# Performance work log

Hardware: AMD Instinct MI355X
Metric: run time of the kernel (lower is better)

Reference implementation:

```python
import jax, jax.numpy as jnp
import numpy as np

D_MODEL = 1024
N_HEADS = 16
D_K = D_MODEL // N_HEADS
D_FF = 4096
THETA = 10000.0
B, S = 2, 2048
EPS = 1e-5


def _trunc_normal(key, shape, fan_in, fan_out):
    std = np.sqrt(2.0 / (fan_in + fan_out))
    return std * jax.random.truncated_normal(key, -3.0, 3.0, shape, dtype=jnp.float32)


def setup_inputs() -> dict:
    key = jax.random.key(0)
    ks = jax.random.split(key, 9)
    x = jax.random.normal(ks[0], (B, S, D_MODEL), dtype=jnp.float32)
    wq = _trunc_normal(ks[1], (D_MODEL, D_MODEL), D_MODEL, D_MODEL)
    wk = _trunc_normal(ks[2], (D_MODEL, D_MODEL), D_MODEL, D_MODEL)
    wv = _trunc_normal(ks[3], (D_MODEL, D_MODEL), D_MODEL, D_MODEL)
    wo = _trunc_normal(ks[4], (D_MODEL, D_MODEL), D_MODEL, D_MODEL)
    w1 = _trunc_normal(ks[5], (D_FF, D_MODEL), D_MODEL, D_FF)
    w2 = _trunc_normal(ks[6], (D_MODEL, D_FF), D_FF, D_MODEL)
    w3 = _trunc_normal(ks[7], (D_FF, D_MODEL), D_MODEL, D_FF)
    g1 = jnp.ones((D_MODEL,), dtype=jnp.float32)
    g2 = jnp.ones((D_MODEL,), dtype=jnp.float32)
    return {"x": x, "wq": wq, "wk": wk, "wv": wv, "wo": wo,
            "w1": w1, "w2": w2, "w3": w3, "g1": g1, "g2": g2}


def _rmsnorm(x, gain):
    xf = x.astype(jnp.float32)
    rms = jnp.sqrt(jnp.mean(xf * xf, axis=-1, keepdims=True) + EPS)
    return (xf / rms * gain).astype(x.dtype)


def _rope(x):
    # x: [B, H, S, D_K]; block-diag 2x2 rotations on consecutive pairs
    s, d = x.shape[-2], x.shape[-1]
    pos = jnp.arange(s, dtype=jnp.float32)  # [S]
    k = jnp.arange(d // 2, dtype=jnp.float32)
    ang = pos[:, None] / (THETA ** (2.0 * k / d))[None, :]  # [S, d/2]
    cos, sin = jnp.cos(ang), jnp.sin(ang)
    xp = x.reshape(*x.shape[:-1], d // 2, 2)
    x0, x1 = xp[..., 0], xp[..., 1]
    r0 = cos * x0 - sin * x1
    r1 = sin * x0 + cos * x1
    return jnp.stack([r0, r1], axis=-1).reshape(x.shape)


def reference(x, wq, wk, wv, wo, w1, w2, w3, g1, g2):
    # --- attention sublayer ---
    h = _rmsnorm(x, g1)
    q = h @ wq.T
    k = h @ wk.T
    v = h @ wv.T
    def split_heads(t):
        b, s, _ = t.shape
        return t.reshape(b, s, N_HEADS, D_K).transpose(0, 2, 1, 3)  # [B,H,S,Dk]
    q, k, v = split_heads(q), split_heads(k), split_heads(v)
    q, k = _rope(q), _rope(k)
    scores = jnp.einsum('bhqd,bhkd->bhqk', q, k) / jnp.sqrt(jnp.float32(D_K))
    s = x.shape[-2]
    causal = jnp.tril(jnp.ones((s, s), dtype=bool))
    scores = jnp.where(causal, scores, -jnp.inf)
    attn = jax.nn.softmax(scores, axis=-1)
    o = jnp.einsum('bhqk,bhkd->bhqd', attn, v)
    o = o.transpose(0, 2, 1, 3).reshape(x.shape[0], s, D_MODEL)
    x = x + o @ wo.T
    # --- SwiGLU FFN sublayer ---
    h2 = _rmsnorm(x, g2)
    a = h2 @ w1.T
    gate = a * jax.nn.sigmoid(a)
    ff = (gate * (h2 @ w3.T)) @ w2.T
    return x + ff
```

## Files before the change

### kernel.cpp

```cpp
#include <hip/hip_runtime.h>
#include <hip/hip_bf16.h>
#include <cstddef>
#include <cstdint>

#define D_MODEL 1024
#define N_HEADS 16
#define D_K     64
#define D_FF    4096
#define BATCH   2
#define SEQ     2048
#define TOKENS  (BATCH * SEQ)
#define EPS     1e-5f

typedef __attribute__((ext_vector_type(8))) short short8;
typedef __attribute__((ext_vector_type(4))) float f32x4;

#define MFMA_BF16 __builtin_amdgcn_mfma_f32_16x16x32_bf16

static __device__ __forceinline__ short f2bf(float f) {
    __hip_bfloat16 h = __float2bfloat16(f);
    short s;
    __builtin_memcpy(&s, &h, 2);
    return s;
}

static __device__ __forceinline__ void async_ld16(const short* g, short* l) {
    __builtin_amdgcn_global_load_lds(
        (const __attribute__((address_space(1))) void*)g,
        (__attribute__((address_space(3))) void*)l,
        16, 0, 0);
}

__global__ __launch_bounds__(256) void cvt_weights(
    const float* wq, const float* wk, const float* wv, const float* wo,
    const float* w1, const float* w3, const float* w2, short* dst)
{
    const size_t M1 = 1 << 20;
    size_t e = ((size_t)blockIdx.x * 256 + threadIdx.x) * 4;
    const float* src;
    size_t off;
    if (e < M1)            { src = wq; off = e; }
    else if (e < 2 * M1)   { src = wk; off = e - M1; }
    else if (e < 3 * M1)   { src = wv; off = e - 2 * M1; }
    else if (e < 4 * M1)   { src = wo; off = e - 3 * M1; }
    else if (e < 12 * M1) {
        size_t r = (e - 4 * M1) >> 10;
        size_t col = e & 1023;
        size_t p = r >> 5, half = (r >> 4) & 1, idx = r & 15;
        src = half ? w3 : w1;
        off = (p * 16 + idx) * 1024 + col;
    }
    else                   { src = w2; off = e - 12 * M1; }
    float4 v = *reinterpret_cast<const float4*>(src + off);
    short4 o;
    o.x = f2bf(v.x); o.y = f2bf(v.y); o.z = f2bf(v.z); o.w = f2bf(v.w);
    *reinterpret_cast<short4*>(dst + e) = o;
}

__global__ __launch_bounds__(256) void rmsnorm_kernel(
    const float* __restrict__ x, const float* __restrict__ g,
    __hip_bfloat16* __restrict__ out)
{
    int row = blockIdx.x;
    int tid = threadIdx.x;
    int lane = tid & 63, wave = tid >> 6;
    const float4* xv = reinterpret_cast<const float4*>(x + (size_t)row * D_MODEL);
    float4 v = xv[tid];
    float ss = v.x * v.x + v.y * v.y + v.z * v.z + v.w * v.w;
#pragma unroll
    for (int m = 1; m < 64; m <<= 1) ss += __shfl_xor(ss, m, 64);
    __shared__ float red[4];
    if (lane == 0) red[wave] = ss;
    __syncthreads();
    float tot = red[0] + red[1] + red[2] + red[3];
    float inv = 1.0f / sqrtf(tot * (1.0f / D_MODEL) + EPS);
    float4 gv = reinterpret_cast<const float4*>(g)[tid];
    size_t base = (size_t)row * D_MODEL + (size_t)tid * 4;
    out[base + 0] = __float2bfloat16(v.x * inv * gv.x);
    out[base + 1] = __float2bfloat16(v.y * inv * gv.y);
    out[base + 2] = __float2bfloat16(v.z * inv * gv.z);
    out[base + 3] = __float2bfloat16(v.w * inv * gv.w);
}

__global__ __launch_bounds__(256) void resid_norm_kernel(
    const float* __restrict__ x, const float* __restrict__ P,
    const float* __restrict__ g, float* __restrict__ out,
    __hip_bfloat16* __restrict__ h)
{
    int row = blockIdx.x;
    int tid = threadIdx.x;
    int lane = tid & 63, wave = tid >> 6;
    size_t base = (size_t)row * D_MODEL + (size_t)tid * 4;
    float4 v  = *reinterpret_cast<const float4*>(x + base);
    float4 p0 = *reinterpret_cast<const float4*>(P + base);
    float4 p1 = *reinterpret_cast<const float4*>(P + (size_t)TOKENS * D_MODEL + base);
    v.x += p0.x + p1.x; v.y += p0.y + p1.y;
    v.z += p0.z + p1.z; v.w += p0.w + p1.w;
    *reinterpret_cast<float4*>(out + base) = v;
    float ss = v.x * v.x + v.y * v.y + v.z * v.z + v.w * v.w;
#pragma unroll
    for (int m = 1; m < 64; m <<= 1) ss += __shfl_xor(ss, m, 64);
    __shared__ float red[4];
    if (lane == 0) red[wave] = ss;
    __syncthreads();
    float tot = red[0] + red[1] + red[2] + red[3];
    float inv = 1.0f / sqrtf(tot * (1.0f / D_MODEL) + EPS);
    float4 gv = reinterpret_cast<const float4*>(g)[tid];
    h[base + 0] = __float2bfloat16(v.x * inv * gv.x);
    h[base + 1] = __float2bfloat16(v.y * inv * gv.y);
    h[base + 2] = __float2bfloat16(v.z * inv * gv.z);
    h[base + 3] = __float2bfloat16(v.w * inv * gv.w);
}

__global__ __launch_bounds__(256) void final_add_kernel(
    float* __restrict__ out, const float* __restrict__ Q)
{
    size_t base = ((size_t)blockIdx.x * 256 + threadIdx.x) * 4;
    float4 v  = *reinterpret_cast<const float4*>(out + base);
    float4 q0 = *reinterpret_cast<const float4*>(Q + base);
    float4 q1 = *reinterpret_cast<const float4*>(Q + (size_t)TOKENS * D_MODEL + base);
    v.x += q0.x + q1.x; v.y += q0.y + q1.y;
    v.z += q0.z + q1.z; v.w += q0.w + q1.w;
    *reinterpret_cast<float4*>(out + base) = v;
}

template<int EPI>
__global__ __launch_bounds__(256) void gemm_bt(
    const short* __restrict__ A, const short* __restrict__ W,
    void* __restrict__ Cout, int K, int lda, int ldc)
{
    __shared__ short Alds[128 * 32];
    __shared__ short Blds[128 * 32];

    const int lane = threadIdx.x & 63;
    const int wv = threadIdx.x >> 6;
    const int quad = lane >> 4, l16 = lane & 15;
    const int wm = wv & 1, wn = wv >> 1;
    const int rowblk = blockIdx.y * 128;
    const int colblk = blockIdx.x * 128;

    const int srow = lane >> 2;
    const int sseg = ((lane & 3) - (lane >> 3)) & 3;
    const short* sA0 = A + (size_t)(rowblk + wv * 16 + srow) * lda + sseg * 8;
    const short* sA1 = A + (size_t)(rowblk + (wv + 4) * 16 + srow) * lda + sseg * 8;
    const short* sB0 = W + (size_t)(colblk + wv * 16 + srow) * (size_t)K + sseg * 8;
    const short* sB1 = W + (size_t)(colblk + (wv + 4) * 16 + srow) * (size_t)K + sseg * 8;
    short* lA0 = &Alds[wv * 512];
    short* lA1 = &Alds[(wv + 4) * 512];
    short* lB0 = &Blds[wv * 512];
    short* lB1 = &Blds[(wv + 4) * 512];

    int aoff[4], boff[4];
#pragma unroll
    for (int i = 0; i < 4; ++i) {
        int tr = wm * 64 + i * 16 + l16;
        aoff[i] = tr * 32 + ((quad + (tr >> 1)) & 3) * 8;
        int tc = wn * 64 + i * 16 + l16;
        boff[i] = tc * 32 + ((quad + (tc >> 1)) & 3) * 8;
    }

    f32x4 acc[4][4];
#pragma unroll
    for (int i = 0; i < 4; ++i)
#pragma unroll
        for (int j = 0; j < 4; ++j)
            acc[i][j] = (f32x4){0.f, 0.f, 0.f, 0.f};

    for (int kk = 0; kk < K; kk += 32) {
        if (kk) __syncthreads();
        async_ld16(sA0 + kk, lA0);
        async_ld16(sA1 + kk, lA1);
        async_ld16(sB0 + kk, lB0);
        async_ld16(sB1 + kk, lB1);
        __syncthreads();
        short8 af[4], bf[4];
#pragma unroll
        for (int i = 0; i < 4; ++i) af[i] = *reinterpret_cast<const short8*>(&Alds[aoff[i]]);
#pragma unroll
        for (int j = 0; j < 4; ++j) bf[j] = *reinterpret_cast<const short8*>(&Blds[boff[j]]);
#pragma unroll
        for (int i = 0; i < 4; ++i)
#pragma unroll
            for (int j = 0; j < 4; ++j)
                acc[i][j] = MFMA_BF16(af[i], bf[j], acc[i][j], 0, 0, 0);
    }

    if (EPI == 2) {
#pragma unroll
        for (int i = 0; i < 4; ++i) {
#pragma unroll
            for (int jp = 0; jp < 2; ++jp) {
#pragma unroll
                for (int r = 0; r < 4; ++r) {
                    int row = rowblk + wm * 64 + i * 16 + quad * 4 + r;
                    int col = blockIdx.x * 64 + wn * 32 + jp * 16 + l16;
                    float a = acc[i][2 * jp][r];
                    float b3 = acc[i][2 * jp + 1][r];
                    float gv = a / (1.f + __expf(-a)) * b3;
                    reinterpret_cast<__hip_bfloat16*>(Cout)[(size_t)row * ldc + col] =
                        __float2bfloat16(gv);
                }
            }
        }
    } else {
#pragma unroll
        for (int i = 0; i < 4; ++i) {
#pragma unroll
            for (int j = 0; j < 4; ++j) {
#pragma unroll
                for (int r = 0; r < 4; ++r) {
                    int row = rowblk + wm * 64 + i * 16 + quad * 4 + r;
                    int col = colblk + wn * 64 + j * 16 + l16;
                    reinterpret_cast<float*>(Cout)[(size_t)row * ldc + col] = acc[i][j][r];
                }
            }
        }
    }
}

template<int SPLIT>
__global__ __launch_bounds__(256) void gemm_bt_sk(
    const short* __restrict__ A, const short* __restrict__ W,
    float* __restrict__ P, int K, int lda, int ldc)
{
    __shared__ short Alds[128 * 32];
    __shared__ short Blds[128 * 32];

    const int Kc = K / SPLIT;
    const int kbase = blockIdx.z * Kc;
    float* Cout = P + (size_t)blockIdx.z * TOKENS * ldc;

    const int lane = threadIdx.x & 63;
    const int wv = threadIdx.x >> 6;
    const int quad = lane >> 4, l16 = lane & 15;
    const int wm = wv & 1, wn = wv >> 1;
    const int rowblk = blockIdx.y * 128;
    const int colblk = blockIdx.x * 128;

    const int srow = lane >> 2;
    const int sseg = ((lane & 3) - (lane >> 3)) & 3;
    const short* sA0 = A + (size_t)(rowblk + wv * 16 + srow) * lda + kbase + sseg * 8;
    const short* sA1 = A + (size_t)(rowblk + (wv + 4) * 16 + srow) * lda + kbase + sseg * 8;
    const short* sB0 = W + (size_t)(colblk + wv * 16 + srow) * (size_t)K + kbase + sseg * 8;
    const short* sB1 = W + (size_t)(colblk + (wv + 4) * 16 + srow) * (size_t)K + kbase + sseg * 8;
    short* lA0 = &Alds[wv * 512];
    short* lA1 = &Alds[(wv + 4) * 512];
    short* lB0 = &Blds[wv * 512];
    short* lB1 = &Blds[(wv + 4) * 512];

    int aoff[4], boff[4];
#pragma unroll
    for (int i = 0; i < 4; ++i) {
        int tr = wm * 64 + i * 16 + l16;
        aoff[i] = tr * 32 + ((quad + (tr >> 1)) & 3) * 8;
        int tc = wn * 64 + i * 16 + l16;
        boff[i] = tc * 32 + ((quad + (tc >> 1)) & 3) * 8;
    }

    f32x4 acc[4][4];
#pragma unroll
    for (int i = 0; i < 4; ++i)
#pragma unroll
        for (int j = 0; j < 4; ++j)
            acc[i][j] = (f32x4){0.f, 0.f, 0.f, 0.f};

    for (int kk = 0; kk < Kc; kk += 32) {
        if (kk) __syncthreads();
        async_ld16(sA0 + kk, lA0);
        async_ld16(sA1 + kk, lA1);
        async_ld16(sB0 + kk, lB0);
        async_ld16(sB1 + kk, lB1);
        __syncthreads();
        short8 af[4], bf[4];
#pragma unroll
        for (int i = 0; i < 4; ++i) af[i] = *reinterpret_cast<const short8*>(&Alds[aoff[i]]);
#pragma unroll
        for (int j = 0; j < 4; ++j) bf[j] = *reinterpret_cast<const short8*>(&Blds[boff[j]]);
#pragma unroll
        for (int i = 0; i < 4; ++i)
#pragma unroll
            for (int j = 0; j < 4; ++j)
                acc[i][j] = MFMA_BF16(af[i], bf[j], acc[i][j], 0, 0, 0);
    }

#pragma unroll
    for (int i = 0; i < 4; ++i) {
#pragma unroll
        for (int j = 0; j < 4; ++j) {
#pragma unroll
            for (int r = 0; r < 4; ++r) {
                int row = rowblk + wm * 64 + i * 16 + quad * 4 + r;
                int col = colblk + wn * 64 + j * 16 + l16;
                Cout[(size_t)row * ldc + col] = acc[i][j][r];
            }
        }
    }
}

__global__ __launch_bounds__(256) void rope_kernel(
    const float* __restrict__ qkv,
    __hip_bfloat16* __restrict__ qb, __hip_bfloat16* __restrict__ kb)
{
    int idx = blockIdx.x * 256 + threadIdx.x;
    int p = idx & 31;
    int h = (idx >> 5) & 15;
    int tok = idx >> 9;
    int s = tok & (SEQ - 1);
    int b = tok >> 11;
    float invf = exp2f((float)p * -(0.03125f * 13.287712379549449f));
    float ang = (float)s * invf;
    float c, sn;
    sincosf(ang, &sn, &c);
    size_t base = (size_t)tok * 3072 + h * 64 + 2 * p;
    float q0 = qkv[base], q1 = qkv[base + 1];
    float k0 = qkv[base + D_MODEL], k1 = qkv[base + D_MODEL + 1];
    float cq = c * 0.125f, sq = sn * 0.125f;
    size_t ob = ((size_t)(b * N_HEADS + h) * SEQ + s) * D_K + 2 * p;
    qb[ob]     = __float2bfloat16(cq * q0 - sq * q1);
    qb[ob + 1] = __float2bfloat16(sq * q0 + cq * q1);
    kb[ob]     = __float2bfloat16(c * k0 - sn * k1);
    kb[ob + 1] = __float2bfloat16(sn * k0 + c * k1);
}

__global__ __launch_bounds__(256) void vtrans_kernel(
    const float* __restrict__ qkv, __hip_bfloat16* __restrict__ vt)
{
    __shared__ float tile[64 * 65];
    const int bh = blockIdx.y;
    const int s0 = blockIdx.x * 64;
    const int t = threadIdx.x;
    const int r = t >> 4, c4 = (t & 15) * 4;
    const float* src = qkv + ((size_t)(bh >> 4) * SEQ + s0) * 3072 + 2048 + (bh & 15) * 64;
#pragma unroll
    for (int p = 0; p < 4; ++p) {
        int s = p * 16 + r;
        float4 v = *reinterpret_cast<const float4*>(src + (size_t)s * 3072 + c4);
        tile[s * 65 + c4 + 0] = v.x;
        tile[s * 65 + c4 + 1] = v.y;
        tile[s * 65 + c4 + 2] = v.z;
        tile[s * 65 + c4 + 3] = v.w;
    }
    __syncthreads();
    const int d = t >> 2, sg = (t & 3) * 16;
    __hip_bfloat16* dst = vt + ((size_t)bh * 64 + d) * SEQ + s0 + sg;
    short8 o0, o1;
#pragma unroll
    for (int i = 0; i < 8; ++i) o0[i] = f2bf(tile[(sg + i) * 65 + d]);
#pragma unroll
    for (int i = 0; i < 8; ++i) o1[i] = f2bf(tile[(sg + 8 + i) * 65 + d]);
    *reinterpret_cast<short8*>(dst) = o0;
    *reinterpret_cast<short8*>(dst + 8) = o1;
}

__global__ __launch_bounds__(256) void attn_kernel(
    const __hip_bfloat16* __restrict__ qbp, const __hip_bfloat16* __restrict__ kbp,
    const __hip_bfloat16* __restrict__ vtp, __hip_bfloat16* __restrict__ o)
{
    const int wave = threadIdx.x >> 6;
    const int lane = threadIdx.x & 63;
    const int quad = lane >> 4, l16 = lane & 15;
    const int bh = blockIdx.y;
    const int t = blockIdx.x + wave * 16;
    const int q0 = t * 32;

    const short* Q  = reinterpret_cast<const short*>(qbp) + ((size_t)bh * SEQ + q0) * D_K;
    const short* Kp = reinterpret_cast<const short*>(kbp) + (size_t)bh * SEQ * D_K;
    const short* Vt = reinterpret_cast<const short*>(vtp) + (size_t)bh * D_K * SEQ;

    short8 qfr[2][2];
#pragma unroll
    for (int f = 0; f < 2; ++f) {
        qfr[f][0] = *reinterpret_cast<const short8*>(Q + (size_t)(f * 16 + l16) * D_K + quad * 8);
        qfr[f][1] = *reinterpret_cast<const short8*>(Q + (size_t)(f * 16 + l16) * D_K + 32 + quad * 8);
    }

    f32x4 oacc[2][4];
    f32x4 lacc[2];
#pragma unroll
    for (int f = 0; f < 2; ++f) {
        lacc[f] = (f32x4){0.f, 0.f, 0.f, 0.f};
#pragma unroll
        for (int g = 0; g < 4; ++g) oacc[f][g] = (f32x4){0.f, 0.f, 0.f, 0.f};
    }

    short8 ones;
#pragma unroll
    for (int i = 0; i < 8; ++i) ones[i] = (short)0x3F80;

    __shared__ short plds[4][32 * 36];
    short* myP = &plds[wave][0];

    for (int kk = 0; kk < q0 + 32; kk += 32) {
        f32x4 sf[2][2];
#pragma unroll
        for (int kg = 0; kg < 2; ++kg) {
            const short* Kr = Kp + (size_t)(kk + kg * 16 + l16) * D_K;
            short8 kf0 = *reinterpret_cast<const short8*>(Kr + quad * 8);
            short8 kf1 = *reinterpret_cast<const short8*>(Kr + 32 + quad * 8);
#pragma unroll
            for (int f = 0; f < 2; ++f) {
                f32x4 z = (f32x4){0.f, 0.f, 0.f, 0.f};
                z = MFMA_BF16(qfr[f][0], kf0, z, 0, 0, 0);
                z = MFMA_BF16(qfr[f][1], kf1, z, 0, 0, 0);
                sf[f][kg] = z;
            }
        }
#pragma unroll
        for (int f = 0; f < 2; ++f) {
            const int qlo = q0 + f * 16;
#pragma unroll
            for (int kg = 0; kg < 2; ++kg) {
                const int keylo = kk + kg * 16;
                const bool needmask = keylo >= qlo;
                const int key = keylo + l16;
#pragma unroll
                for (int r = 0; r < 4; ++r) {
                    float p = __expf(sf[f][kg][r]);
                    if (needmask) {
                        int qrow = qlo + quad * 4 + r;
                        p = (key > qrow) ? 0.f : p;
                    }
                    myP[(f * 16 + quad * 4 + r) * 36 + keylo - kk + l16] = f2bf(p);
                }
            }
        }
        asm volatile("s_waitcnt lgkmcnt(0)" ::: "memory");
        short8 pf[2];
#pragma unroll
        for (int f = 0; f < 2; ++f) {
            pf[f] = *reinterpret_cast<const short8*>(&myP[(f * 16 + l16) * 36 + quad * 8]);
            lacc[f] = MFMA_BF16(pf[f], ones, lacc[f], 0, 0, 0);
        }
#pragma unroll
        for (int g = 0; g < 4; ++g) {
            short8 vf = *reinterpret_cast<const short8*>(
                Vt + (size_t)(g * 16 + l16) * SEQ + kk + quad * 8);
#pragma unroll
            for (int f = 0; f < 2; ++f)
                oacc[f][g] = MFMA_BF16(pf[f], vf, oacc[f][g], 0, 0, 0);
        }
    }

    const int b = bh >> 4, h = bh & 15;
#pragma unroll
    for (int f = 0; f < 2; ++f) {
#pragma unroll
        for (int g = 0; g < 4; ++g) {
#pragma unroll
            for (int r = 0; r < 4; ++r) {
                int qrow = q0 + f * 16 + quad * 4 + r;
                float v = oacc[f][g][r] / lacc[f][r];
                o[(size_t)(b * SEQ + qrow) * D_MODEL + h * 64 + g * 16 + l16] =
                    __float2bfloat16(v);
            }
        }
    }
}

extern "C" void kernel_launch(void* const* d_in, const int* in_sizes, int n_in,
                              void* d_out, int out_size, void* d_ws, size_t ws_size,
                              hipStream_t stream)
{
    const float* x  = (const float*)d_in[0];
    const float* wq = (const float*)d_in[1];
    const float* wk = (const float*)d_in[2];
    const float* wv = (const float*)d_in[3];
    const float* wo = (const float*)d_in[4];
    const float* w1 = (const float*)d_in[5];
    const float* w2 = (const float*)d_in[6];
    const float* w3 = (const float*)d_in[7];
    const float* g1 = (const float*)d_in[8];
    const float* g2 = (const float*)d_in[9];
    float* out = (float*)d_out;

    char* ws = (char*)d_ws;
    const size_t OFF_WTS  = 0;
    const size_t OFF_H    = 33554432;
    const size_t OFF_QKV  = 41943040;
    const size_t OFF_QB   = 92274688;
    const size_t OFF_KB   = 100663296;
    const size_t OFF_VT   = 109051904;
    const size_t OFF_O    = 117440512;
    const size_t OFF_P    = OFF_QKV;
    const size_t OFF_GATE = OFF_QKV;
    const size_t OFF_Q2   = OFF_QB;

    short* wts  = (short*)(ws + OFF_WTS);
    short* wqkvb = wts;
    short* wob  = wts + (size_t)3 * (1 << 20);
    short* w13b = wts + (size_t)4 * (1 << 20);
    short* w2b  = wts + (size_t)12 * (1 << 20);
    __hip_bfloat16* h  = (__hip_bfloat16*)(ws + OFF_H);
    float* qkv = (float*)(ws + OFF_QKV);
    __hip_bfloat16* qb = (__hip_bfloat16*)(ws + OFF_QB);
    __hip_bfloat16* kb = (__hip_bfloat16*)(ws + OFF_KB);
    __hip_bfloat16* vt = (__hip_bfloat16*)(ws + OFF_VT);
    __hip_bfloat16* ob = (__hip_bfloat16*)(ws + OFF_O);
    float* Pwo  = (float*)(ws + OFF_P);
    __hip_bfloat16* gate = (__hip_bfloat16*)(ws + OFF_GATE);
    float* Qw2  = (float*)(ws + OFF_Q2);

    cvt_weights<<<16384, 256, 0, stream>>>(wq, wk, wv, wo, w1, w3, w2, wts);
    rmsnorm_kernel<<<TOKENS, 256, 0, stream>>>(x, g1, h);
    gemm_bt<0><<<dim3(3072 / 128, TOKENS / 128), 256, 0, stream>>>(
        (const short*)h, wqkvb, qkv, D_MODEL, D_MODEL, 3072);
    rope_kernel<<<8192, 256, 0, stream>>>(qkv, qb, kb);
    vtrans_kernel<<<dim3(SEQ / 64, BATCH * N_HEADS), 256, 0, stream>>>(qkv, vt);
    attn_kernel<<<dim3(16, BATCH * N_HEADS), 256, 0, stream>>>(qb, kb, vt, ob);
    gemm_bt_sk<2><<<dim3(D_MODEL / 128, TOKENS / 128, 2), 256, 0, stream>>>(
        (const short*)ob, wob, Pwo, D_MODEL, D_MODEL, D_MODEL);
    resid_norm_kernel<<<TOKENS, 256, 0, stream>>>(x, Pwo, g2, out, h);
    gemm_bt<2><<<dim3(8192 / 128, TOKENS / 128), 256, 0, stream>>>(
        (const short*)h, w13b, gate, D_MODEL, D_MODEL, D_FF);
    gemm_bt_sk<2><<<dim3(D_MODEL / 128, TOKENS / 128, 2), 256, 0, stream>>>(
        (const short*)gate, w2b, Qw2, D_FF, D_FF, D_MODEL);
    final_add_kernel<<<TOKENS * D_MODEL / 1024, 256, 0, stream>>>(out, Qw2);
    (void)in_sizes; (void)n_in; (void)out_size; (void)ws_size;
}
```

Before: 429.6 us.

## Double GEMM K-step to 64 and store QKV projection as bf16

The GEMM kernels now stage a 64-wide K slice per iteration, issuing two async loads per operand into a doubled LDS buffer. This halves the number of barrier pairs per K loop. Separately, the QKV projection writes bf16 instead of fp32 through a new epilogue variant, and the rope and V-transpose kernels read bf16. That halves the intermediate traffic, at the cost of rounding Q/K/V to bf16 before RoPE, which adds a small precision loss.

```diff
diff --git a/kernel.cpp b/kernel.cpp
--- a/kernel.cpp
+++ b/kernel.cpp
@@ -22,6 +22,11 @@
     short s;
     __builtin_memcpy(&s, &h, 2);
     return s;
+}
+static __device__ __forceinline__ float bf2f(short s) {
+    __hip_bfloat16 h;
+    __builtin_memcpy(&h, &s, 2);
+    return __bfloat162float(h);
 }
 
 static __device__ __forceinline__ void async_ld16(const short* g, short* l) {
@@ -129,8 +134,8 @@
     const short* __restrict__ A, const short* __restrict__ W,
     void* __restrict__ Cout, int K, int lda, int ldc)
 {
-    __shared__ short Alds[128 * 32];
-    __shared__ short Blds[128 * 32];
+    __shared__ short Alds[128 * 64];
+    __shared__ short Blds[128 * 64];
 
     const int lane = threadIdx.x & 63;
     const int wv = threadIdx.x >> 6;
@@ -166,23 +171,32 @@
         for (int j = 0; j < 4; ++j)
             acc[i][j] = (f32x4){0.f, 0.f, 0.f, 0.f};
 
-    for (int kk = 0; kk < K; kk += 32) {
+    for (int kk = 0; kk < K; kk += 64) {
         if (kk) __syncthreads();
         async_ld16(sA0 + kk, lA0);
         async_ld16(sA1 + kk, lA1);
         async_ld16(sB0 + kk, lB0);
         async_ld16(sB1 + kk, lB1);
+        async_ld16(sA0 + kk + 32, lA0 + 4096);
+        async_ld16(sA1 + kk + 32, lA1 + 4096);
+        async_ld16(sB0 + kk + 32, lB0 + 4096);
+        async_ld16(sB1 + kk + 32, lB1 + 4096);
         __syncthreads();
-        short8 af[4], bf[4];
-#pragma unroll
-        for (int i = 0; i < 4; ++i) af[i] = *reinterpret_cast<const short8*>(&Alds[aoff[i]]);
-#pragma unroll
-        for (int j = 0; j < 4; ++j) bf[j] = *reinterpret_cast<const short8*>(&Blds[boff[j]]);
-#pragma unroll
-        for (int i = 0; i < 4; ++i)
+#pragma unroll
+        for (int hf = 0; hf < 2; ++hf) {
+            short8 af[4], bf[4];
+#pragma unroll
+            for (int i = 0; i < 4; ++i)
+                af[i] = *reinterpret_cast<const short8*>(&Alds[hf * 4096 + aoff[i]]);
 #pragma unroll
             for (int j = 0; j < 4; ++j)
-                acc[i][j] = MFMA_BF16(af[i], bf[j], acc[i][j], 0, 0, 0);
+                bf[j] = *reinterpret_cast<const short8*>(&Blds[hf * 4096 + boff[j]]);
+#pragma unroll
+            for (int i = 0; i < 4; ++i)
+#pragma unroll
+                for (int j = 0; j < 4; ++j)
+                    acc[i][j] = MFMA_BF16(af[i], bf[j], acc[i][j], 0, 0, 0);
+        }
     }
 
     if (EPI == 2) {
@@ -211,7 +225,12 @@
                 for (int r = 0; r < 4; ++r) {
                     int row = rowblk + wm * 64 + i * 16 + quad * 4 + r;
                     int col = colblk + wn * 64 + j * 16 + l16;
-                    reinterpret_cast<float*>(Cout)[(size_t)row * ldc + col] = acc[i][j][r];
+                    size_t idx = (size_t)row * ldc + col;
+                    if (EPI == 3)
+                        reinterpret_cast<__hip_bfloat16*>(Cout)[idx] =
+                            __float2bfloat16(acc[i][j][r]);
+                    else
+                        reinterpret_cast<float*>(Cout)[idx] = acc[i][j][r];
                 }
             }
         }
@@ -223,8 +242,8 @@
     const short* __restrict__ A, const short* __restrict__ W,
     float* __restrict__ P, int K, int lda, int ldc)
 {
-    __shared__ short Alds[128 * 32];
-    __shared__ short Blds[128 * 32];
+    __shared__ short Alds[128 * 64];
+    __shared__ short Blds[128 * 64];
 
     const int Kc = K / SPLIT;
     const int kbase = blockIdx.z * Kc;
@@ -264,23 +283,32 @@
         for (int j = 0; j < 4; ++j)
             acc[i][j] = (f32x4){0.f, 0.f, 0.f, 0.f};
 
-    for (int kk = 0; kk < Kc; kk += 32) {
+    for (int kk = 0; kk < Kc; kk += 64) {
         if (kk) __syncthreads();
         async_ld16(sA0 + kk, lA0);
         async_ld16(sA1 + kk, lA1);
         async_ld16(sB0 + kk, lB0);
         async_ld16(sB1 + kk, lB1);
+        async_ld16(sA0 + kk + 32, lA0 + 4096);
+        async_ld16(sA1 + kk + 32, lA1 + 4096);
+        async_ld16(sB0 + kk + 32, lB0 + 4096);
+        async_ld16(sB1 + kk + 32, lB1 + 4096);
         __syncthreads();
-        short8 af[4], bf[4];
-#pragma unroll
-        for (int i = 0; i < 4; ++i) af[i] = *reinterpret_cast<const short8*>(&Alds[aoff[i]]);
-#pragma unroll
-        for (int j = 0; j < 4; ++j) bf[j] = *reinterpret_cast<const short8*>(&Blds[boff[j]]);
-#pragma unroll
-        for (int i = 0; i < 4; ++i)
+#pragma unroll
+        for (int hf = 0; hf < 2; ++hf) {
+            short8 af[4], bf[4];
+#pragma unroll
+            for (int i = 0; i < 4; ++i)
+                af[i] = *reinterpret_cast<const short8*>(&Alds[hf * 4096 + aoff[i]]);
 #pragma unroll
             for (int j = 0; j < 4; ++j)
-                acc[i][j] = MFMA_BF16(af[i], bf[j], acc[i][j], 0, 0, 0);
+                bf[j] = *reinterpret_cast<const short8*>(&Blds[hf * 4096 + boff[j]]);
+#pragma unroll
+            for (int i = 0; i < 4; ++i)
+#pragma unroll
+                for (int j = 0; j < 4; ++j)
+                    acc[i][j] = MFMA_BF16(af[i], bf[j], acc[i][j], 0, 0, 0);
+        }
     }
 
 #pragma unroll
@@ -298,7 +326,7 @@
 }
 
 __global__ __launch_bounds__(256) void rope_kernel(
-    const float* __restrict__ qkv,
+    const short* __restrict__ qk,
     __hip_bfloat16* __restrict__ qb, __hip_bfloat16* __restrict__ kb)
 {
     int idx = blockIdx.x * 256 + threadIdx.x;
@@ -312,8 +340,8 @@
     float c, sn;
     sincosf(ang, &sn, &c);
     size_t base = (size_t)tok * 3072 + h * 64 + 2 * p;
-    float q0 = qkv[base], q1 = qkv[base + 1];
-    float k0 = qkv[base + D_MODEL], k1 = qkv[base + D_MODEL + 1];
+    float q0 = bf2f(qk[base]),           q1 = bf2f(qk[base + 1]);
+    float k0 = bf2f(qk[base + D_MODEL]), k1 = bf2f(qk[base + D_MODEL + 1]);
     float cq = c * 0.125f, sq = sn * 0.125f;
     size_t ob = ((size_t)(b * N_HEADS + h) * SEQ + s) * D_K + 2 * p;
     qb[ob]     = __float2bfloat16(cq * q0 - sq * q1);
@@ -323,22 +351,22 @@
 }
 
 __global__ __launch_bounds__(256) void vtrans_kernel(
-    const float* __restrict__ qkv, __hip_bfloat16* __restrict__ vt)
+    const short* __restrict__ qk, __hip_bfloat16* __restrict__ vt)
 {
     __shared__ float tile[64 * 65];
     const int bh = blockIdx.y;
     const int s0 = blockIdx.x * 64;
     const int t = threadIdx.x;
     const int r = t >> 4, c4 = (t & 15) * 4;
-    const float* src = qkv + ((size_t)(bh >> 4) * SEQ + s0) * 3072 + 2048 + (bh & 15) * 64;
+    const short* src = qk + ((size_t)(bh >> 4) * SEQ + s0) * 3072 + 2048 + (bh & 15) * 64;
 #pragma unroll
     for (int p = 0; p < 4; ++p) {
         int s = p * 16 + r;
-        float4 v = *reinterpret_cast<const float4*>(src + (size_t)s * 3072 + c4);
-        tile[s * 65 + c4 + 0] = v.x;
-        tile[s * 65 + c4 + 1] = v.y;
-        tile[s * 65 + c4 + 2] = v.z;
-        tile[s * 65 + c4 + 3] = v.w;
+        short4 v = *reinterpret_cast<const short4*>(src + (size_t)s * 3072 + c4);
+        tile[s * 65 + c4 + 0] = bf2f(v.x);
+        tile[s * 65 + c4 + 1] = bf2f(v.y);
+        tile[s * 65 + c4 + 2] = bf2f(v.z);
+        tile[s * 65 + c4 + 3] = bf2f(v.w);
     }
     __syncthreads();
     const int d = t >> 2, sg = (t & 3) * 16;
@@ -491,7 +519,7 @@
     short* w13b = wts + (size_t)4 * (1 << 20);
     short* w2b  = wts + (size_t)12 * (1 << 20);
     __hip_bfloat16* h  = (__hip_bfloat16*)(ws + OFF_H);
-    float* qkv = (float*)(ws + OFF_QKV);
+    short* qkvb = (short*)(ws + OFF_QKV);
     __hip_bfloat16* qb = (__hip_bfloat16*)(ws + OFF_QB);
     __hip_bfloat16* kb = (__hip_bfloat16*)(ws + OFF_KB);
     __hip_bfloat16* vt = (__hip_bfloat16*)(ws + OFF_VT);
@@ -502,10 +530,10 @@
 
     cvt_weights<<<16384, 256, 0, stream>>>(wq, wk, wv, wo, w1, w3, w2, wts);
     rmsnorm_kernel<<<TOKENS, 256, 0, stream>>>(x, g1, h);
-    gemm_bt<0><<<dim3(3072 / 128, TOKENS / 128), 256, 0, stream>>>(
-        (const short*)h, wqkvb, qkv, D_MODEL, D_MODEL, 3072);
-    rope_kernel<<<8192, 256, 0, stream>>>(qkv, qb, kb);
-    vtrans_kernel<<<dim3(SEQ / 64, BATCH * N_HEADS), 256, 0, stream>>>(qkv, vt);
+    gemm_bt<3><<<dim3(3072 / 128, TOKENS / 128), 256, 0, stream>>>(
+        (const short*)h, wqkvb, qkvb, D_MODEL, D_MODEL, 3072);
+    rope_kernel<<<8192, 256, 0, stream>>>(qkvb, qb, kb);
+    vtrans_kernel<<<dim3(SEQ / 64, BATCH * N_HEADS), 256, 0, stream>>>(qkvb, vt);
     attn_kernel<<<dim3(16, BATCH * N_HEADS), 256, 0, stream>>>(qb, kb, vt, ob);
     gemm_bt_sk<2><<<dim3(D_MODEL / 128, TOKENS / 128, 2), 256, 0, stream>>>(
         (const short*)ob, wob, Pwo, D_MODEL, D_MODEL, D_MODEL);
```

New measurement: 420.9 us. 2.0% less time.
